# Performance work log

Hardware: AMD Instinct MI355X
Metric: run time of the kernel (lower is better)

The kernel has to match this reference:

```python
import jax, jax.numpy as jnp
import numpy as np

B, T, N, F = 16, 12, 1000, 64
K_CHEB, OUT = 3, 64


def setup_inputs() -> dict:
    key = jax.random.key(0)
    k1, k2, k3, k4 = jax.random.split(key, 4)
    x = jax.random.normal(k1, (B, T, N, F), dtype=jnp.float32)
    SAtt = jax.random.uniform(k2, (B, N, N), dtype=jnp.float32)
    cheb = jax.random.normal(k3, (K_CHEB, N, N), dtype=jnp.float32) * 0.05
    Theta = jax.random.normal(k4, (K_CHEB, F, OUT), dtype=jnp.float32) * 0.05
    return {"x": x, "SAtt": SAtt, "cheb": cheb, "Theta": Theta}


def reference(x, SAtt, cheb, Theta):
    # Attention-masked Chebyshev polynomials: A[b,k,i,j] = cheb[k,i,j] * SAtt[b,i,j]
    A = cheb[None, :, :, :] * SAtt[:, None, :, :]          # (B,K,N,N)
    # rhs[b,t,k,i,f] = sum_j A[b,k,j,i] * x[b,t,j,f]  (transpose of A in original code)
    rhs = jnp.einsum('bkji,btjf->btkif', A, x)             # (B,T,K,N,F)
    # accumulate over k with per-k feature transform Theta[k]
    out = jnp.einsum('btkif,kfo->btio', rhs, Theta)        # (B,T,N,OUT)
    return jax.nn.relu(out)
```

## Files before the change

### kernel.cpp

```cpp
#include <hip/hip_runtime.h>

#define B_  16
#define T_  12
#define N_  1000
#define F_  64
#define KC  3
#define O_  64
#define NP  1024
#define KP  (KC * NP)
#define CC  (T_ * O_)

typedef __bf16 bf16x8 __attribute__((ext_vector_type(8)));
typedef float  f32x4  __attribute__((ext_vector_type(4)));

__device__ __forceinline__ unsigned short f2bf(float f) {
  __bf16 h = (__bf16)f;
  return __builtin_bit_cast(unsigned short, h);
}

__device__ __forceinline__ void gl_lds16(const void* g, void* l) {
  __builtin_amdgcn_global_load_lds(
      (const __attribute__((address_space(1))) unsigned int*)g,
      (__attribute__((address_space(3))) unsigned int*)l,
      16, 0, 0);
}

__global__ __launch_bounds__(256) void k_build_as(
    const float* __restrict__ SAtt, const float* __restrict__ cheb,
    unsigned short* __restrict__ ASt) {
  __shared__ unsigned short prod[KC][64][65];
  const int tid = threadIdx.x;
  const int b = blockIdx.z, ib = blockIdx.x * 64, jb = blockIdx.y * 64;

  const int ii = tid & 63, j0 = tid >> 6;
  for (int p = 0; p < 16; ++p) {
    const int jj = p * 4 + j0;
    const int gi = ib + ii, gj = jb + jj;
    const bool ok = (gi < N_) && (gj < N_);
    const int gic = gi < N_ ? gi : N_ - 1;
    const int gjc = gj < N_ ? gj : N_ - 1;
    const float s = SAtt[(size_t)(b * N_ + gjc) * N_ + gic];
#pragma unroll
    for (int k = 0; k < KC; ++k) {
      const float c = cheb[(size_t)(k * N_ + gjc) * N_ + gic];
      prod[k][jj][ii] = ok ? f2bf(s * c) : (unsigned short)0;
    }
  }
  __syncthreads();

  const int jq = (tid & 15) * 4, i0 = tid >> 4;
  for (int p = 0; p < 4; ++p) {
    const int iw = p * 16 + i0;
#pragma unroll
    for (int k = 0; k < KC; ++k) {
      ushort4 v;
      v.x = prod[k][jq + 0][iw];
      v.y = prod[k][jq + 1][iw];
      v.z = prod[k][jq + 2][iw];
      v.w = prod[k][jq + 3][iw];
      *(ushort4*)&ASt[((size_t)(b * NP + ib + iw) * KC + k) * NP + (jb + jq)] = v;
    }
  }
}

__global__ __launch_bounds__(256) void k_build_y(
    const float* __restrict__ x, const float* __restrict__ Theta,
    unsigned short* __restrict__ Yt) {
  __shared__ unsigned short thl[KC][64][72];
  __shared__ unsigned short xl[128][72];
  const int tid = threadIdx.x;
  const int bt = blockIdx.y;
  const int jb = blockIdx.x * 128;

  for (int idx = tid; idx < KC * F_ * O_; idx += 256) {
    const int k = idx >> 12, f = (idx >> 6) & 63, o = idx & 63;
    thl[k][o][f] = f2bf(Theta[idx]);
  }
  const float* xrow = x + ((size_t)bt * N_ + jb) * F_;
  for (int p = 0; p < 8; ++p) {
    const int i4 = tid + p * 256;
    const int fl = i4 * 4, j = fl >> 6, f = fl & 63;
    float4 v;
    if (jb + j < N_) v = ((const float4*)xrow)[i4];
    else             v = make_float4(0.f, 0.f, 0.f, 0.f);
    ushort4 u;
    u.x = f2bf(v.x); u.y = f2bf(v.y); u.z = f2bf(v.z); u.w = f2bf(v.w);
    *(ushort4*)&xl[j][f] = u;
  }
  __syncthreads();

  const int w = tid >> 6, l = tid & 63, quad = l >> 4, lr = l & 15;
#pragma unroll
  for (int k = 0; k < KC; ++k) {
    f32x4 acc[4][2];
#pragma unroll
    for (int mi = 0; mi < 4; ++mi)
#pragma unroll
      for (int ni = 0; ni < 2; ++ni)
        acc[mi][ni] = (f32x4){0.f, 0.f, 0.f, 0.f};
#pragma unroll
    for (int ks = 0; ks < 2; ++ks) {
      const int fo = ks * 32 + quad * 8;
      bf16x8 a[4], bb[2];
#pragma unroll
      for (int mi = 0; mi < 4; ++mi)
        a[mi] = *(const bf16x8*)&thl[k][mi * 16 + lr][fo];
#pragma unroll
      for (int ni = 0; ni < 2; ++ni)
        bb[ni] = *(const bf16x8*)&xl[w * 32 + ni * 16 + lr][fo];
#pragma unroll
      for (int mi = 0; mi < 4; ++mi)
#pragma unroll
        for (int ni = 0; ni < 2; ++ni)
          acc[mi][ni] = __builtin_amdgcn_mfma_f32_16x16x32_bf16(
              a[mi], bb[ni], acc[mi][ni], 0, 0, 0);
    }
#pragma unroll
    for (int mi = 0; mi < 4; ++mi)
#pragma unroll
      for (int ni = 0; ni < 2; ++ni)
#pragma unroll
        for (int r = 0; r < 4; ++r) {
          const int o = mi * 16 + quad * 4 + r;
          const int j = jb + w * 32 + ni * 16 + lr;
          Yt[((size_t)(bt * O_ + o) * KC + k) * NP + j] = f2bf(acc[mi][ni][r]);
        }
  }
}

__global__ __launch_bounds__(256, 2) void k_gemm(
    const unsigned short* __restrict__ ASt, const unsigned short* __restrict__ Yt,
    float* __restrict__ out) {
  __shared__ unsigned short Al[128 * 64];
  __shared__ unsigned short Bl[128 * 64];
  const int tid = threadIdx.x;
  const int b = blockIdx.z, ib = blockIdx.y * 128, cb = blockIdx.x * 128;
  const unsigned short* Abase = ASt + ((size_t)b * NP + ib) * KP;
  const unsigned short* Bbase = Yt + ((size_t)b * CC + cb) * KP;
  const int w = tid >> 6, l = tid & 63, quad = l >> 4, lr = l & 15;
  const int wr = w & 1, wc = w >> 1;
  const int lrow = l >> 3, lchunk = l & 7;

  f32x4 acc[4][4];
#pragma unroll
  for (int mi = 0; mi < 4; ++mi)
#pragma unroll
    for (int ci = 0; ci < 4; ++ci)
      acc[mi][ci] = (f32x4){0.f, 0.f, 0.f, 0.f};

  for (int kt = 0; kt < KP / 64; ++kt) {
    __syncthreads();
    const int k0 = kt * 64;
#pragma unroll
    for (int s = 0; s < 4; ++s) {
      const int row = w * 32 + s * 8;
      gl_lds16(Abase + (size_t)(row + lrow) * KP + k0 + lchunk * 8, &Al[row * 64]);
      gl_lds16(Bbase + (size_t)(row + lrow) * KP + k0 + lchunk * 8, &Bl[row * 64]);
    }
    __syncthreads();
#pragma unroll
    for (int ks = 0; ks < 2; ++ks) {
      const int ko = ks * 32 + quad * 8;
      bf16x8 a[4], bb[4];
#pragma unroll
      for (int mi = 0; mi < 4; ++mi)
        a[mi] = *(const bf16x8*)&Al[(wr * 64 + mi * 16 + lr) * 64 + ko];
#pragma unroll
      for (int ci = 0; ci < 4; ++ci)
        bb[ci] = *(const bf16x8*)&Bl[(wc * 64 + ci * 16 + lr) * 64 + ko];
#pragma unroll
      for (int mi = 0; mi < 4; ++mi)
#pragma unroll
        for (int ci = 0; ci < 4; ++ci)
          acc[mi][ci] = __builtin_amdgcn_mfma_f32_16x16x32_bf16(
              a[mi], bb[ci], acc[mi][ci], 0, 0, 0);
    }
  }

#pragma unroll
  for (int mi = 0; mi < 4; ++mi) {
    const int i = ib + wr * 64 + mi * 16 + quad * 4;
#pragma unroll
    for (int ci = 0; ci < 4; ++ci) {
      const int c = cb + wc * 64 + ci * 16 + lr;
      const int t = c >> 6, o = c & 63;
#pragma unroll
      for (int r = 0; r < 4; ++r) {
        if (i + r < N_) {
          const float v = acc[mi][ci][r];
          out[((size_t)(b * T_ + t) * N_ + (i + r)) * O_ + o] = v > 0.f ? v : 0.f;
        }
      }
    }
  }
}

extern "C" void kernel_launch(void* const* d_in, const int* in_sizes, int n_in,
                              void* d_out, int out_size, void* d_ws, size_t ws_size,
                              hipStream_t stream) {
  const float* x     = (const float*)d_in[0];
  const float* SAtt  = (const float*)d_in[1];
  const float* cheb  = (const float*)d_in[2];
  const float* Theta = (const float*)d_in[3];
  float* out = (float*)d_out;

  unsigned short* ASt = (unsigned short*)d_ws;
  unsigned short* Yt  = ASt + (size_t)B_ * NP * KC * NP;

  k_build_as<<<dim3(16, 16, B_), 256, 0, stream>>>(SAtt, cheb, ASt);
  k_build_y<<<dim3(8, B_ * T_), 256, 0, stream>>>(x, Theta, Yt);
  k_gemm<<<dim3(CC / 128, NP / 128, B_), 256, 0, stream>>>(ASt, Yt, out);
}
```

Before: 378.4 us.

## Swizzle GEMM LDS, remap blocks per XCD, vectorize build kernels' global accesses

The GEMM applies an XOR swizzle to LDS chunk placement to remove bank conflicts on bf16x8 reads. It also flattens the grid so each XCD handles whole batches, improving L2 reuse of A and B tiles. The build kernels switch to float4 loads and wide 16-byte stores, with Yt writes staged through an LDS transpose. This adds extra LDS usage and syncs in build_y.

Measured after the change: 321.8 us. 1.18x faster.

```diff
diff --git a/kernel.cpp b/kernel.cpp
--- a/kernel.cpp
+++ b/kernel.cpp
@@ -28,37 +28,47 @@
 __global__ __launch_bounds__(256) void k_build_as(
     const float* __restrict__ SAtt, const float* __restrict__ cheb,
     unsigned short* __restrict__ ASt) {
-  __shared__ unsigned short prod[KC][64][65];
+  __shared__ unsigned short prod[KC][64][66];
   const int tid = threadIdx.x;
   const int b = blockIdx.z, ib = blockIdx.x * 64, jb = blockIdx.y * 64;
 
-  const int ii = tid & 63, j0 = tid >> 6;
-  for (int p = 0; p < 16; ++p) {
-    const int jj = p * 4 + j0;
-    const int gi = ib + ii, gj = jb + jj;
-    const bool ok = (gi < N_) && (gj < N_);
-    const int gic = gi < N_ ? gi : N_ - 1;
+  const int ii4 = (tid & 15) * 4, jr = tid >> 4;
+#pragma unroll
+  for (int p = 0; p < 4; ++p) {
+    const int jj = p * 16 + jr;
+    const int gj = jb + jj;
     const int gjc = gj < N_ ? gj : N_ - 1;
-    const float s = SAtt[(size_t)(b * N_ + gjc) * N_ + gic];
+    const int gi = ib + ii4;
+    const bool iok = gi < N_;
+    const bool ok = iok && (gj < N_);
+    float4 s4 = make_float4(0.f, 0.f, 0.f, 0.f);
+    if (iok) s4 = *(const float4*)&SAtt[((size_t)b * N_ + gjc) * N_ + gi];
 #pragma unroll
     for (int k = 0; k < KC; ++k) {
-      const float c = cheb[(size_t)(k * N_ + gjc) * N_ + gic];
-      prod[k][jj][ii] = ok ? f2bf(s * c) : (unsigned short)0;
+      float4 c4 = make_float4(0.f, 0.f, 0.f, 0.f);
+      if (iok) c4 = *(const float4*)&cheb[((size_t)k * N_ + gjc) * N_ + gi];
+      ushort2 lo, hi;
+      lo.x = ok ? f2bf(c4.x * s4.x) : (unsigned short)0;
+      lo.y = ok ? f2bf(c4.y * s4.y) : (unsigned short)0;
+      hi.x = ok ? f2bf(c4.z * s4.z) : (unsigned short)0;
+      hi.y = ok ? f2bf(c4.w * s4.w) : (unsigned short)0;
+      *(ushort2*)&prod[k][jj][ii4]     = lo;
+      *(ushort2*)&prod[k][jj][ii4 + 2] = hi;
     }
   }
   __syncthreads();
 
-  const int jq = (tid & 15) * 4, i0 = tid >> 4;
-  for (int p = 0; p < 4; ++p) {
-    const int iw = p * 16 + i0;
+  const int j8 = (tid & 7) * 8, i0 = tid >> 3;
+#pragma unroll
+  for (int p = 0; p < 2; ++p) {
+    const int iw = p * 32 + i0;
 #pragma unroll
     for (int k = 0; k < KC; ++k) {
-      ushort4 v;
-      v.x = prod[k][jq + 0][iw];
-      v.y = prod[k][jq + 1][iw];
-      v.z = prod[k][jq + 2][iw];
-      v.w = prod[k][jq + 3][iw];
-      *(ushort4*)&ASt[((size_t)(b * NP + ib + iw) * KC + k) * NP + (jb + jq)] = v;
+      unsigned short v[8];
+#pragma unroll
+      for (int m = 0; m < 8; ++m) v[m] = prod[k][j8 + m][iw];
+      *(uint4*)&ASt[((size_t)(b * NP + ib + iw) * KC + k) * NP + jb + j8] =
+          *(uint4*)v;
     }
   }
 }
@@ -68,15 +78,23 @@
     unsigned short* __restrict__ Yt) {
   __shared__ unsigned short thl[KC][64][72];
   __shared__ unsigned short xl[128][72];
+  __shared__ unsigned short ot[64][136];
   const int tid = threadIdx.x;
   const int bt = blockIdx.y;
   const int jb = blockIdx.x * 128;
 
-  for (int idx = tid; idx < KC * F_ * O_; idx += 256) {
-    const int k = idx >> 12, f = (idx >> 6) & 63, o = idx & 63;
-    thl[k][o][f] = f2bf(Theta[idx]);
+#pragma unroll
+  for (int it = 0; it < 12; ++it) {
+    const int e = (tid + it * 256) * 4;
+    const int k = e >> 12, f = (e >> 6) & 63, o0 = e & 63;
+    const float4 v = *(const float4*)&Theta[e];
+    thl[k][o0 + 0][f] = f2bf(v.x);
+    thl[k][o0 + 1][f] = f2bf(v.y);
+    thl[k][o0 + 2][f] = f2bf(v.z);
+    thl[k][o0 + 3][f] = f2bf(v.w);
   }
   const float* xrow = x + ((size_t)bt * N_ + jb) * F_;
+#pragma unroll
   for (int p = 0; p < 8; ++p) {
     const int i4 = tid + p * 256;
     const int fl = i4 * 4, j = fl >> 6, f = fl & 63;
@@ -90,6 +108,7 @@
   __syncthreads();
 
   const int w = tid >> 6, l = tid & 63, quad = l >> 4, lr = l & 15;
+  const int o16 = tid >> 4, j8v = (tid & 15) * 8;
 #pragma unroll
   for (int k = 0; k < KC; ++k) {
     f32x4 acc[4][2];
@@ -115,16 +134,22 @@
           acc[mi][ni] = __builtin_amdgcn_mfma_f32_16x16x32_bf16(
               a[mi], bb[ni], acc[mi][ni], 0, 0, 0);
     }
+    __syncthreads();
 #pragma unroll
     for (int mi = 0; mi < 4; ++mi)
 #pragma unroll
       for (int ni = 0; ni < 2; ++ni)
 #pragma unroll
-        for (int r = 0; r < 4; ++r) {
-          const int o = mi * 16 + quad * 4 + r;
-          const int j = jb + w * 32 + ni * 16 + lr;
-          Yt[((size_t)(bt * O_ + o) * KC + k) * NP + j] = f2bf(acc[mi][ni][r]);
-        }
+        for (int r = 0; r < 4; ++r)
+          ot[mi * 16 + quad * 4 + r][w * 32 + ni * 16 + lr] =
+              f2bf(acc[mi][ni][r]);
+    __syncthreads();
+#pragma unroll
+    for (int oo = 0; oo < 4; ++oo) {
+      const int o = oo * 16 + o16;
+      const uint4 v = *(const uint4*)&ot[o][j8v];
+      *(uint4*)&Yt[((size_t)(bt * O_ + o) * KC + k) * NP + jb + j8v] = v;
+    }
   }
 }
 
@@ -134,12 +159,19 @@
   __shared__ unsigned short Al[128 * 64];
   __shared__ unsigned short Bl[128 * 64];
   const int tid = threadIdx.x;
-  const int b = blockIdx.z, ib = blockIdx.y * 128, cb = blockIdx.x * 128;
+  const int bid = blockIdx.x;
+  const int xcd = bid & 7, s = bid >> 3;
+  const int b = xcd * 2 + (s / 48);
+  const int r48 = s % 48;
+  const int ib = (r48 / 6) * 128, cb = (r48 % 6) * 128;
+
   const unsigned short* Abase = ASt + ((size_t)b * NP + ib) * KP;
   const unsigned short* Bbase = Yt + ((size_t)b * CC + cb) * KP;
   const int w = tid >> 6, l = tid & 63, quad = l >> 4, lr = l & 15;
   const int wr = w & 1, wc = w >> 1;
   const int lrow = l >> 3, lchunk = l & 7;
+  const int src_chunk = lchunk ^ lrow;
+  const int p0 = quad ^ (lr & 7);
 
   f32x4 acc[4][4];
 #pragma unroll
@@ -152,22 +184,24 @@
     __syncthreads();
     const int k0 = kt * 64;
 #pragma unroll
-    for (int s = 0; s < 4; ++s) {
-      const int row = w * 32 + s * 8;
-      gl_lds16(Abase + (size_t)(row + lrow) * KP + k0 + lchunk * 8, &Al[row * 64]);
-      gl_lds16(Bbase + (size_t)(row + lrow) * KP + k0 + lchunk * 8, &Bl[row * 64]);
+    for (int s4 = 0; s4 < 4; ++s4) {
+      const int row = w * 32 + s4 * 8;
+      gl_lds16(Abase + (size_t)(row + lrow) * KP + k0 + src_chunk * 8,
+               &Al[row * 64]);
+      gl_lds16(Bbase + (size_t)(row + lrow) * KP + k0 + src_chunk * 8,
+               &Bl[row * 64]);
     }
     __syncthreads();
 #pragma unroll
     for (int ks = 0; ks < 2; ++ks) {
-      const int ko = ks * 32 + quad * 8;
+      const int pc = (p0 ^ (ks * 4)) * 8;
       bf16x8 a[4], bb[4];
 #pragma unroll
       for (int mi = 0; mi < 4; ++mi)
-        a[mi] = *(const bf16x8*)&Al[(wr * 64 + mi * 16 + lr) * 64 + ko];
+        a[mi] = *(const bf16x8*)&Al[(wr * 64 + mi * 16 + lr) * 64 + pc];
 #pragma unroll
       for (int ci = 0; ci < 4; ++ci)
-        bb[ci] = *(const bf16x8*)&Bl[(wc * 64 + ci * 16 + lr) * 64 + ko];
+        bb[ci] = *(const bf16x8*)&Bl[(wc * 64 + ci * 16 + lr) * 64 + pc];
 #pragma unroll
       for (int mi = 0; mi < 4; ++mi)
 #pragma unroll
@@ -209,5 +243,5 @@
 
   k_build_as<<<dim3(16, 16, B_), 256, 0, stream>>>(SAtt, cheb, ASt);
   k_build_y<<<dim3(8, B_ * T_), 256, 0, stream>>>(x, Theta, Yt);
-  k_gemm<<<dim3(CC / 128, NP / 128, B_), 256, 0, stream>>>(ASt, Yt, out);
-}
+  k_gemm<<<768, 256, 0, stream>>>(ASt, Yt, out);
+}
```
